# Optimization experiments

Measured on AMD Instinct MI355X. Metric: run time of the kernel, lower is better.

## Reference

```python
import jax, jax.numpy as jnp
import numpy as np
from jax import lax

V, E, H, B, S, L, T = 30000, 300, 256, 32, 256, 4, 9
H2 = 2 * H            # bidirectional encoder output / decoder hidden
DIN = 2 * H2 + L      # decoder LSTM input size


def setup_inputs() -> dict:
    key = jax.random.key(0)
    ks = jax.random.split(key, 14)
    rn = lambda k, shp, s=0.05: (jax.random.normal(k, shp, dtype=jnp.float32) * s)
    return {
        "seqs": jax.random.randint(ks[0], (B, S), 0, V, dtype=jnp.int32),
        "emb": rn(ks[1], (V, E)),
        "enc_Wih_f": rn(ks[2], (4 * H, E)),
        "enc_Whh_f": rn(ks[3], (4 * H, H)),
        "enc_b_f": rn(ks[4], (4 * H,)),
        "enc_Wih_b": rn(ks[5], (4 * H, E)),
        "enc_Whh_b": rn(ks[6], (4 * H, H)),
        "enc_b_b": rn(ks[7], (4 * H,)),
        "W_att": rn(ks[8], (H2, H2)),
        "dec_Wih": rn(ks[9], (4 * H2, DIN)),
        "dec_Whh": rn(ks[10], (4 * H2, H2)),
        "dec_b": rn(ks[11], (4 * H2,)),
        "W_tag": rn(ks[12], (T, H2)),
        "b_tag": rn(ks[13], (T,)),
    }


def _lstm_scan(x_seq, Wih, Whh, b, hidden):
    """x_seq: [S,B,Din] -> outputs [S,B,hidden]. PyTorch gate order i,f,g,o."""
    nb = x_seq.shape[1]
    h0 = jnp.zeros((nb, hidden), x_seq.dtype)
    c0 = jnp.zeros((nb, hidden), x_seq.dtype)

    def step(carry, x):
        h, c = carry
        g = x @ Wih.T + h @ Whh.T + b
        i, f, gg, o = jnp.split(g, 4, axis=-1)
        c = jax.nn.sigmoid(f) * c + jax.nn.sigmoid(i) * jnp.tanh(gg)
        h = jax.nn.sigmoid(o) * jnp.tanh(c)
        return (h, c), h

    _, hs = lax.scan(step, (h0, c0), x_seq)
    return hs


def reference(seqs, emb, enc_Wih_f, enc_Whh_f, enc_b_f, enc_Wih_b, enc_Whh_b,
              enc_b_b, W_att, dec_Wih, dec_Whh, dec_b, W_tag, b_tag):
    # embed and transpose to [S, B, E]
    x = jnp.transpose(emb[seqs], (1, 0, 2))
    # bidirectional encoder LSTM -> h: [S, B, 2H]
    h_f = _lstm_scan(x, enc_Wih_f, enc_Whh_f, enc_b_f, H)
    h_b = jnp.flip(_lstm_scan(jnp.flip(x, 0), enc_Wih_b, enc_Whh_b, enc_b_b, H), 0)
    h = jnp.concatenate([h_f, h_b], axis=-1)

    # precompute W_att @ h (same math as per-step linear in original)
    Wh = jnp.einsum('sbh,oh->sbo', h, W_att)   # [S,B,H2]

    s0 = jnp.zeros((B, H2), x.dtype)
    c0 = jnp.zeros((B, H2), x.dtype)

    def decode_level(carry, onehot):           # onehot: [L]
        def step(carry2, h_t):                 # h_t: [B,H2]
            s, c = carry2
            score = jnp.einsum('sbo,bo->bs', Wh, s)       # [B,S]
            att = jax.nn.softmax(score, axis=1)
            ctx = jnp.einsum('sbh,bs->bh', h, att)        # [B,H2]
            xin = jnp.concatenate(
                [ctx, h_t, jnp.broadcast_to(onehot, (B, L))], axis=-1)
            g = xin @ dec_Wih.T + s @ dec_Whh.T + dec_b
            i, f, gg, o = jnp.split(g, 4, axis=-1)
            c = jax.nn.sigmoid(f) * c + jax.nn.sigmoid(i) * jnp.tanh(gg)
            s = jax.nn.sigmoid(o) * jnp.tanh(c)
            return (s, c), s

        carry, outs = lax.scan(step, carry, h)  # outs: [S,B,H2]
        return carry, outs

    # state (s,c) persists across nested levels, matching the original loop
    _, all_outs = lax.scan(decode_level, (s0, c0), jnp.eye(L, dtype=x.dtype))
    # [L,S,B,H2] -> tag scores [L,S,B,T]
    return jnp.einsum('lsbh,th->lsbt', all_outs, W_tag) + b_tag
```

## Files before the change

kernel.cpp:

```cpp
#include <hip/hip_runtime.h>
#include <cstdint>
#include <cstddef>

using u16 = unsigned short;
using u32 = unsigned int;

typedef __attribute__((ext_vector_type(8))) __bf16 bf16x8;
typedef __attribute__((ext_vector_type(4))) float f32x4;

__device__ __forceinline__ float bf2f(u16 u){
  union { u32 i; float f; } v; v.i = ((u32)u) << 16; return v.f;
}
__device__ __forceinline__ u16 f2bf(float f){
  union { float f; u32 i; } v; v.f = f;
  return (u16)((v.i + 0x7FFFu + ((v.i >> 16) & 1u)) >> 16);
}
__device__ __forceinline__ float sigm(float x){ return 1.0f / (1.0f + __expf(-x)); }
__device__ __forceinline__ f32x4 mfma16(bf16x8 a, bf16x8 b, f32x4 c){
  return __builtin_amdgcn_mfma_f32_16x16x32_bf16(a, b, c, 0, 0, 0);
}
__device__ __forceinline__ float ldin(const void* p, size_t i, bool f){
  return f ? ((const float*)p)[i] : bf2f(((const u16*)p)[i]);
}

__device__ __forceinline__ void gbar(u32* bar, u32 target){
  __syncthreads();
  if (threadIdx.x == 0){
    __hip_atomic_fetch_add(bar, 1u, __ATOMIC_ACQ_REL, __HIP_MEMORY_SCOPE_AGENT);
    while (__hip_atomic_load(bar, __ATOMIC_RELAXED, __HIP_MEMORY_SCOPE_AGENT) < target)
      __builtin_amdgcn_s_sleep(2);
    (void)__hip_atomic_load(bar, __ATOMIC_ACQUIRE, __HIP_MEMORY_SCOPE_AGENT);
  }
  __syncthreads();
}

__global__ __launch_bounds__(256) void k_detect(const u32* __restrict__ embw, u32* __restrict__ dflag){
  int tid = threadIdx.x;
  u32 cnt = 0;
  for (int t = 0; t < 32; ++t){
    u32 w = embw[t*256 + tid];
    u32 e = (w >> 7) & 0xFFu;
    cnt += (e >= 0xC0u) ? 1u : 0u;
  }
  atomicAdd(dflag, cnt);
}


__global__ __launch_bounds__(256) void k_pack(
  const void* eWihF, const void* eWihB, const void* ebF, const void* ebB,
  const void* dWih, const void* dWhh, const void* db, const void* Wtag,
  const void* eWhhF, const void* eWhhB, const void* Watt, const void* btag,
  const u32* __restrict__ dflag,
  u16* __restrict__ WihCat, float* __restrict__ bcat, u16* __restrict__ WihH,
  u16* __restrict__ Wf, float* __restrict__ lbv, u16* __restrict__ WtagP,
  u16* __restrict__ WhhFb, u16* __restrict__ WhhBb, u16* __restrict__ Wattb,
  float* __restrict__ btagf)
{
  bool isf = (*dflag > 64u);
  long i = (long)blockIdx.x * 256 + threadIdx.x;
  if (i < 655360){
    long n = i / 320, e = i - n*320;
    WihCat[i] = (e < 300)
      ? f2bf(ldin(n < 1024 ? eWihF : eWihB, (size_t)(n & 1023)*300 + e, isf)) : (u16)0;
    return;
  }
  i -= 655360;
  if (i < 2048){ bcat[i] = ldin(i < 1024 ? ebF : ebB, (size_t)(i & 1023), isf); return; }
  i -= 2048;
  if (i < 1048576){
    long n = i >> 9, k = i & 511;
    WihH[i] = f2bf(ldin(dWih, (size_t)n*1028 + 512 + k, isf));
    return;
  }
  i -= 1048576;
  if (i < 2097152){
    long e  = i & 7;
    long ln = (i >> 3) & 63;
    long kt = (i >> 9) & 31;
    long rt = (i >> 14) & 3;
    long wgi = i >> 16;
    long n = rt*512 + wgi*16 + (ln & 15);
    long k = kt*32 + (ln >> 4)*8 + e;
    Wf[i] = f2bf((k < 512) ? ldin(dWih, (size_t)n*1028 + k, isf)
                           : ldin(dWhh, (size_t)n*512 + (k - 512), isf));
    return;
  }
  i -= 2097152;
  if (i < 8192){
    long l = i >> 11, n = i & 2047;
    lbv[i] = ldin(db, n, isf) + ldin(dWih, (size_t)n*1028 + 1024 + l, isf);
    return;
  }
  i -= 8192;
  if (i < 8192){
    long n = i >> 9, k = i & 511;
    WtagP[i] = (n < 9) ? f2bf(ldin(Wtag, (size_t)n*512 + k, isf)) : (u16)0;
    return;
  }
  i -= 8192;
  if (i < 262144){ WhhFb[i] = f2bf(ldin(eWhhF, i, isf)); return; }
  i -= 262144;
  if (i < 262144){ WhhBb[i] = f2bf(ldin(eWhhB, i, isf)); return; }
  i -= 262144;
  if (i < 262144){ Wattb[i] = f2bf(ldin(Watt, i, isf)); return; }
  i -= 262144;
  if (i < 16){ btagf[i] = (i < 9) ? ldin(btag, i, isf) : 0.f; return; }
}

__global__ __launch_bounds__(256) void k_gather(
  const int* __restrict__ seqs, const void* __restrict__ emb,
  const u32* __restrict__ dflag, u16* __restrict__ X)
{
  bool isf = (*dflag > 64u);
  int idx = blockIdx.x * 256 + threadIdx.x;
  if (idx >= 8192*320) return;
  int row = idx / 320, e = idx - row*320;
  int s = row >> 5, b = row & 31;
  int tok = seqs[b*256 + s];
  X[idx] = (e < 300) ? f2bf(ldin(emb, (size_t)tok*300 + e, isf)) : (u16)0;
}


__global__ __launch_bounds__(256) void k_gemm(
  const u16* __restrict__ A, const u16* __restrict__ B, const float* __restrict__ bias,
  u16* __restrict__ C, int M, int N, int K)
{
  int mb = blockIdx.x * 32;
  int wave = threadIdx.x >> 6, lane = threadIdx.x & 63;
  int nb = blockIdx.y * 256 + wave * 64;
  int rlo = lane & 15, klane = (lane >> 4) * 8;
  f32x4 acc[2][4];
  #pragma unroll
  for (int i = 0; i < 2; ++i)
    #pragma unroll
    for (int j = 0; j < 4; ++j) acc[i][j] = (f32x4){0,0,0,0};
  for (int kk = 0; kk < K; kk += 32){
    bf16x8 a0 = *(const bf16x8*)(A + (size_t)(mb + rlo)*K + kk + klane);
    bf16x8 a1 = *(const bf16x8*)(A + (size_t)(mb + 16 + rlo)*K + kk + klane);
    #pragma unroll
    for (int nt = 0; nt < 4; ++nt){
      bf16x8 bv = *(const bf16x8*)(B + (size_t)(nb + nt*16 + rlo)*K + kk + klane);
      acc[0][nt] = mfma16(a0, bv, acc[0][nt]);
      acc[1][nt] = mfma16(a1, bv, acc[1][nt]);
    }
  }
  int rbase = (lane >> 4) * 4;
  #pragma unroll
  for (int mt = 0; mt < 2; ++mt)
    #pragma unroll
    for (int nt = 0; nt < 4; ++nt){
      int col = nb + nt*16 + rlo;
      float badd = bias ? bias[col] : 0.0f;
      #pragma unroll
      for (int r = 0; r < 4; ++r){
        int row = mb + mt*16 + rbase + r;
        C[(size_t)row*N + col] = f2bf(acc[mt][nt][r] + badd);
      }
    }
}


__global__ __launch_bounds__(256) void k_transp(const u16* __restrict__ hglob, u16* __restrict__ hT)
{
  __shared__ u16 tile_t[64][264];
  int b = blockIdx.x >> 3, d0 = (blockIdx.x & 7) * 64;
  int t = threadIdx.x;
  for (int rr = 0; rr < 16; ++rr){
    int c = rr*256 + t;
    int j = c >> 4, dq = (c & 15) * 4;
    ushort4 ld = *(const ushort4*)(hglob + ((size_t)(j*32 + b)*512 + d0 + dq));
    tile_t[dq + 0][j] = ld.x;
    tile_t[dq + 1][j] = ld.y;
    tile_t[dq + 2][j] = ld.z;
    tile_t[dq + 3][j] = ld.w;
  }
  __syncthreads();
  for (int rr = 0; rr < 8; ++rr){
    int c = rr*256 + t;
    int d = c >> 5, jq = (c & 31) * 8;
    *(uint4*)(hT + ((size_t)(b*512 + d0 + d)*256 + jq)) = *(const uint4*)&tile_t[d][jq];
  }
}


__global__ __launch_bounds__(256, 1) void k_encoder(
  const u16* __restrict__ XW, const u16* __restrict__ WhhF, const u16* __restrict__ WhhB,
  u16* __restrict__ hglob, u16* __restrict__ hstate, float* __restrict__ cstate, u32* ctrl)
{
  int wg = blockIdx.x;
  int d = wg >> 4, w = wg & 15;
  const u16* Whh = d ? WhhB : WhhF;
  float* cst = cstate + d * (32*256);
  u32* bar = ctrl + d * 64;
  int tid = threadIdx.x, wave = tid >> 6, lane = tid & 63;
  int cc = lane & 15, klane = (lane >> 4) * 8, rbase = (lane >> 4) * 4;
  __shared__ float g_lds[4][32][16];
  u32 gen = 0;
  for (int t = 0; t < 256; ++t){
    int srow = d ? (255 - t) : t;
    const u16* hr = hstate + (size_t)(d*2 + (t & 1)) * (32*256);
    u16*       hw = hstate + (size_t)(d*2 + ((t & 1) ^ 1)) * (32*256);
    {
      int ncol = wave*256 + w*16 + cc;
      const u16* Brow = Whh + (size_t)ncol*256;
      f32x4 acc0 = {0,0,0,0}, acc1 = {0,0,0,0};
      #pragma unroll
      for (int kk = 0; kk < 256; kk += 32){
        bf16x8 bv = *(const bf16x8*)(Brow + kk + klane);
        bf16x8 a0 = *(const bf16x8*)(hr + cc*256 + kk + klane);
        bf16x8 a1 = *(const bf16x8*)(hr + (cc + 16)*256 + kk + klane);
        acc0 = mfma16(a0, bv, acc0);
        acc1 = mfma16(a1, bv, acc1);
      }
      #pragma unroll
      for (int r = 0; r < 4; ++r){
        g_lds[wave][rbase + r][cc]      = acc0[r];
        g_lds[wave][16 + rbase + r][cc] = acc1[r];
      }
    }
    __syncthreads();
    for (int e = tid; e < 512; e += 256){
      int b_ = e >> 4, jc = e & 15;
      int j = w*16 + jc;
      float pre[4];
      #pragma unroll
      for (int g2 = 0; g2 < 4; ++g2)
        pre[g2] = g_lds[g2][b_][jc] + bf2f(XW[(size_t)(srow*32 + b_)*2048 + d*1024 + g2*256 + j]);
      float iv = sigm(pre[0]), fv = sigm(pre[1]);
      float gv = tanhf(pre[2]), ov = sigm(pre[3]);
      float cv = fv * cst[b_*256 + j] + iv * gv;
      cst[b_*256 + j] = cv;
      float hv = ov * tanhf(cv);
      u16 hb = f2bf(hv);
      hw[b_*256 + j] = hb;
      hglob[(size_t)(srow*32 + b_)*512 + d*256 + j] = hb;
    }
    gen++;
    gbar(bar, gen * 16u);
  }
}


__global__ __launch_bounds__(512, 1) void k_decoder(
  const u16* __restrict__ Whb, const u16* __restrict__ hT,
  const u16* __restrict__ Wf, const u16* __restrict__ Xh, const float* __restrict__ lbv,
  u16* __restrict__ Ain,
  u16* __restrict__ aouts,
  u32* bar1, u32* bar2)
{
  __shared__ __align__(16) u16 s_stage[512];
  __shared__ float score_lds[256];
  __shared__ __align__(16) u16 att_bf[256];
  __shared__ float gbuf[4][16][33];
  __shared__ float c_lds[512];
  const int wg = blockIdx.x, tid = threadIdx.x;
  const int wave = tid >> 6, lane = tid & 63;
  const int q = lane >> 4, cc = lane & 15;
  c_lds[tid] = 0.0f;

  bf16x8 wh[2][16];
  #pragma unroll
  for (int rt = 0; rt < 2; ++rt)
    #pragma unroll
    for (int kt = 0; kt < 16; ++kt){
      int row = wave*32 + rt*16 + cc;
      wh[rt][kt] = *(const bf16x8*)(Whb + ((size_t)(row*32 + wg))*512 + kt*32 + q*8);
    }
  const int grt = wave >> 1, gct = wave & 1;
  const int bcol = gct*16 + cc;
  const u16* WfW = Wf + (size_t)wg*65536;
  __syncthreads();

  for (int iter = 0; iter < 1024; ++iter){
    const int l = iter >> 8, t = iter & 255;
    u16* AinC = Ain + (iter & 1)*32768;
    u16* AinN = Ain + ((iter & 1) ^ 1)*32768;

    if (tid < 64) ((uint4*)s_stage)[tid] = ((const uint4*)(AinC + wg*1024 + 512))[tid];
    __syncthreads();

    f32x4 sa0 = {0,0,0,0}, sa1 = {0,0,0,0};
    #pragma unroll
    for (int kt = 0; kt < 16; ++kt){
      bf16x8 sv = *(const bf16x8*)(s_stage + kt*32 + q*8);
      sa0 = mfma16(wh[0][kt], sv, sa0);
      sa1 = mfma16(wh[1][kt], sv, sa1);
    }
    if (cc == 0){
      #pragma unroll
      for (int r = 0; r < 4; ++r){
        score_lds[wave*32      + q*4 + r] = sa0[r];
        score_lds[wave*32 + 16 + q*4 + r] = sa1[r];
      }
    }
    __syncthreads();

    if (wave == 0){
      float x0 = score_lds[lane*4+0], x1 = score_lds[lane*4+1];
      float x2 = score_lds[lane*4+2], x3 = score_lds[lane*4+3];
      float m = fmaxf(fmaxf(x0,x1), fmaxf(x2,x3));
      #pragma unroll
      for (int off = 32; off >= 1; off >>= 1) m = fmaxf(m, __shfl_xor(m, off));
      float e0 = __expf(x0-m), e1 = __expf(x1-m), e2 = __expf(x2-m), e3 = __expf(x3-m);
      float s = e0+e1+e2+e3;
      #pragma unroll
      for (int off = 32; off >= 1; off >>= 1) s += __shfl_xor(s, off);
      float inv = 1.0f / s;
      att_bf[lane*4+0] = f2bf(e0*inv);
      att_bf[lane*4+1] = f2bf(e1*inv);
      att_bf[lane*4+2] = f2bf(e2*inv);
      att_bf[lane*4+3] = f2bf(e3*inv);
    }
    __syncthreads();

    f32x4 ca0 = {0,0,0,0}, ca1 = {0,0,0,0}, ca2 = {0,0,0,0}, ca3 = {0,0,0,0};
    #pragma unroll
    for (int jt = 0; jt < 8; ++jt){
      uint4 au = {0,0,0,0};
      if (cc == 0) au = *(const uint4*)(att_bf + jt*32 + q*8);
      bf16x8 af = *(bf16x8*)&au;
      const u16* hb = hT + ((size_t)(wg*512 + wave*64 + cc))*256 + jt*32 + q*8;
      ca0 = mfma16(af, *(const bf16x8*)(hb +    0*256), ca0);
      ca1 = mfma16(af, *(const bf16x8*)(hb +   16*256), ca1);
      ca2 = mfma16(af, *(const bf16x8*)(hb +   32*256), ca2);
      ca3 = mfma16(af, *(const bf16x8*)(hb +   48*256), ca3);
    }
    if (lane < 16){
      AinC[wg*1024 + wave*64 +  0 + lane] = f2bf(ca0[0]);
      AinC[wg*1024 + wave*64 + 16 + lane] = f2bf(ca1[0]);
      AinC[wg*1024 + wave*64 + 32 + lane] = f2bf(ca2[0]);
      AinC[wg*1024 + wave*64 + 48 + lane] = f2bf(ca3[0]);
    }
    __syncthreads();
    if (tid == 0)
      __hip_atomic_fetch_add(bar2, 1u, __ATOMIC_ACQ_REL, __HIP_MEMORY_SCOPE_AGENT);

    f32x4 ga = {0,0,0,0};
    #pragma unroll
    for (int kt = 16; kt < 32; ++kt){
      bf16x8 wa = *(const bf16x8*)(WfW + ((grt*32 + kt)*64 + lane)*8);
      bf16x8 av = *(const bf16x8*)(AinC + bcol*1024 + kt*32 + q*8);
      ga = mfma16(wa, av, ga);
    }
    if (tid == 0){
      const u32 tgt = 32u*(u32)(iter+1);
      while (__hip_atomic_load(bar2, __ATOMIC_RELAXED, __HIP_MEMORY_SCOPE_AGENT) < tgt)
        __builtin_amdgcn_s_sleep(2);
      (void)__hip_atomic_load(bar2, __ATOMIC_ACQUIRE, __HIP_MEMORY_SCOPE_AGENT);
    }
    __syncthreads();
    #pragma unroll
    for (int kt = 0; kt < 16; ++kt){
      bf16x8 wa = *(const bf16x8*)(WfW + ((grt*32 + kt)*64 + lane)*8);
      bf16x8 av = *(const bf16x8*)(AinC + bcol*1024 + kt*32 + q*8);
      ga = mfma16(wa, av, ga);
    }
    #pragma unroll
    for (int r = 0; r < 4; ++r) gbuf[grt][q*4 + r][bcol] = ga[r];
    __syncthreads();

    {
      const int b_ = tid >> 4, dd = tid & 15;
      const int gj = wg*16 + dd;
      float pre[4];
      #pragma unroll
      for (int g = 0; g < 4; ++g){
        int n = g*512 + gj;
        pre[g] = gbuf[g][dd][b_] + bf2f(Xh[(size_t)(t*32 + b_)*2048 + n]) + lbv[l*2048 + n];
      }
      float iv = sigm(pre[0]), fv = sigm(pre[1]);
      float gv = tanhf(pre[2]), ov = sigm(pre[3]);
      float cv = fv * c_lds[tid] + iv * gv;
      c_lds[tid] = cv;
      u16 hb = f2bf(ov * tanhf(cv));
      AinN[b_*1024 + 512 + gj] = hb;
      aouts[(size_t)((l*256 + t)*32 + b_)*512 + gj] = hb;
    }
    __syncthreads();
    if (tid == 0){
      __hip_atomic_fetch_add(bar1, 1u, __ATOMIC_ACQ_REL, __HIP_MEMORY_SCOPE_AGENT);
      const u32 tgt = 32u*(u32)(iter+1);
      while (__hip_atomic_load(bar1, __ATOMIC_RELAXED, __HIP_MEMORY_SCOPE_AGENT) < tgt)
        __builtin_amdgcn_s_sleep(2);
      (void)__hip_atomic_load(bar1, __ATOMIC_ACQUIRE, __HIP_MEMORY_SCOPE_AGENT);
    }
    __syncthreads();
  }
}


__global__ __launch_bounds__(256) void k_tag(
  const u16* __restrict__ aouts, const u16* __restrict__ WtagP, const float* __restrict__ btagf,
  const u32* __restrict__ dflag, void* __restrict__ out)
{
  bool isf = (*dflag > 64u);
  int wave = threadIdx.x >> 6, lane = threadIdx.x & 63;
  int mb = (blockIdx.x * 4 + wave) * 16;
  int cc = lane & 15, klane = (lane >> 4) * 8;
  f32x4 acc = {0,0,0,0};
  const u16* Arow = aouts + (size_t)(mb + cc)*512;
  const u16* Brow = WtagP + cc*512;
  #pragma unroll
  for (int kk = 0; kk < 512; kk += 32){
    bf16x8 av = *(const bf16x8*)(Arow + kk + klane);
    bf16x8 bv = *(const bf16x8*)(Brow + kk + klane);
    acc = mfma16(av, bv, acc);
  }
  int rbase = (lane >> 4) * 4;
  if (cc < 9){
    float bt = btagf[cc];
    #pragma unroll
    for (int r = 0; r < 4; ++r){
      int row = mb + rbase + r;
      float v = acc[r] + bt;
      if (isf) ((float*)out)[(size_t)row*9 + cc] = v;
      else     ((u16*)out)[(size_t)row*9 + cc] = f2bf(v);
    }
  }
}


extern "C" void kernel_launch(void* const* d_in, const int* in_sizes, int n_in,
                              void* d_out, int out_size, void* d_ws, size_t ws_size,
                              hipStream_t stream)
{
  (void)in_sizes; (void)n_in; (void)out_size;
  if (ws_size < 98625536ull) return;

  const int* seqs = (const int*)d_in[0];

  char* ws = (char*)d_ws;
  u32*    ctrl   = (u32*)(ws + 0);
  u32*    dflag  = ctrl + 240;
  u16*    Ain    = (u16*)(ws + 1024);
  u16*    hstate = (u16*)(ws + 132096);
  float*  enc_c  = (float*)(ws + 197632);
  u16*    WihCat = (u16*)(ws + 263168);
  float*  bcat   = (float*)(ws + 1573888);
  u16*    WihH   = (u16*)(ws + 1582080);
  u16*    Wf     = (u16*)(ws + 3679232);
  float*  lbv    = (float*)(ws + 7873536);
  u16*    WtagP  = (u16*)(ws + 7906304);
  u16*    WhhFb  = (u16*)(ws + 7922688);
  u16*    WhhBb  = (u16*)(ws + 8446976);
  u16*    Wattb  = (u16*)(ws + 8971264);
  float*  btagf  = (float*)(ws + 9495552);
  u16*    X      = (u16*)(ws + 9496576);
  u16*    XWXh   = (u16*)(ws + 14739456);
  u16*    aouts  = (u16*)(ws + 48293888);
  u16*    hglob  = (u16*)(ws + 48293888);
  u16*    hT     = (u16*)(ws + 81848320);
  u16*    Whb    = (u16*)(ws + 90236928);

  hipMemsetAsync(d_ws, 0, 263168, stream);

  k_detect<<<1, 256, 0, stream>>>((const u32*)d_in[1], dflag);
  k_pack<<<17993, 256, 0, stream>>>(
      d_in[2], d_in[5], d_in[4], d_in[7], d_in[9], d_in[10], d_in[11], d_in[12],
      d_in[3], d_in[6], d_in[8], d_in[13], dflag,
      WihCat, bcat, WihH, Wf, lbv, WtagP, WhhFb, WhhBb, Wattb, btagf);
  k_gather<<<10240, 256, 0, stream>>>(seqs, d_in[1], dflag, X);
  k_gemm<<<dim3(256, 8), 256, 0, stream>>>(X, WihCat, bcat, XWXh, 8192, 2048, 320);
  k_encoder<<<32, 256, 0, stream>>>(XWXh, WhhFb, WhhBb, hglob, hstate, enc_c, ctrl);
  k_gemm<<<dim3(256, 2), 256, 0, stream>>>(hglob, Wattb, nullptr, Whb, 8192, 512, 512);
  k_gemm<<<dim3(256, 8), 256, 0, stream>>>(hglob, WihH, nullptr, XWXh, 8192, 2048, 512);
  k_transp<<<256, 256, 0, stream>>>(hglob, hT);

  k_decoder<<<32, 512, 0, stream>>>(Whb, hT, Wf, XWXh, lbv, Ain, aouts,
                                    ctrl + 128, ctrl + 160);
  k_tag<<<512, 256, 0, stream>>>(aouts, WtagP, btagf, dflag, d_out);
}
```

Before: 26.47 ms.

## Use relaxed barriers with cache-bypassing loads/stores and LDS staging in recurrent kernels

Replaces acquire/release grid barriers with relaxed atomics plus explicit cache-bypassing (sc0 sc1) global loads and stores and a vmcnt wait, so cross-workgroup state exchange no longer needs full cache invalidation/writeback. The per-step hidden state and decoder input are staged into XOR-swizzled LDS blocks instead of being read repeatedly from global memory. Encoder cell state moves from global into shared memory, and outputs use nontemporal stores. The risk is memory-ordering correctness depending on the hand-written cache-bypass asm, and the decoder now needs 64KB of dynamic LDS.

```diff
diff --git a/kernel.cpp b/kernel.cpp
--- a/kernel.cpp
+++ b/kernel.cpp
@@ -23,15 +23,22 @@
   return f ? ((const float*)p)[i] : bf2f(((const u16*)p)[i]);
 }
 
-__device__ __forceinline__ void gbar(u32* bar, u32 target){
-  __syncthreads();
-  if (threadIdx.x == 0){
-    __hip_atomic_fetch_add(bar, 1u, __ATOMIC_ACQ_REL, __HIP_MEMORY_SCOPE_AGENT);
-    while (__hip_atomic_load(bar, __ATOMIC_RELAXED, __HIP_MEMORY_SCOPE_AGENT) < target)
-      __builtin_amdgcn_s_sleep(2);
-    (void)__hip_atomic_load(bar, __ATOMIC_ACQUIRE, __HIP_MEMORY_SCOPE_AGENT);
-  }
-  __syncthreads();
+__device__ __forceinline__ uint4 ldx4_cg(const u16* p){
+  uint4 r;
+  asm volatile("global_load_dwordx4 %0, %1, off sc0 sc1" : "=v"(r) : "v"(p) : "memory");
+  return r;
+}
+__device__ __forceinline__ void st16_cg(u16* p, u32 v){
+  asm volatile("global_store_short %0, %1, off sc0 sc1" :: "v"(p), "v"(v) : "memory");
+}
+__device__ __forceinline__ void wait_vm0(){ asm volatile("s_waitcnt vmcnt(0)" ::: "memory"); }
+
+__device__ __forceinline__ void bar_arrive(u32* bar){
+  __hip_atomic_fetch_add(bar, 1u, __ATOMIC_RELAXED, __HIP_MEMORY_SCOPE_AGENT);
+}
+__device__ __forceinline__ void bar_spin(u32* bar, u32 tgt){
+  while (__hip_atomic_load(bar, __ATOMIC_RELAXED, __HIP_MEMORY_SCOPE_AGENT) < tgt)
+    __builtin_amdgcn_s_sleep(1);
 }
 
 __global__ __launch_bounds__(256) void k_detect(const u32* __restrict__ embw, u32* __restrict__ dflag){
@@ -185,30 +192,48 @@
 
 __global__ __launch_bounds__(256, 1) void k_encoder(
   const u16* __restrict__ XW, const u16* __restrict__ WhhF, const u16* __restrict__ WhhB,
-  u16* __restrict__ hglob, u16* __restrict__ hstate, float* __restrict__ cstate, u32* ctrl)
+  u16* __restrict__ hglob, u16* __restrict__ hstate, u32* ctrl)
 {
   int wg = blockIdx.x;
   int d = wg >> 4, w = wg & 15;
   const u16* Whh = d ? WhhB : WhhF;
-  float* cst = cstate + d * (32*256);
   u32* bar = ctrl + d * 64;
   int tid = threadIdx.x, wave = tid >> 6, lane = tid & 63;
-  int cc = lane & 15, klane = (lane >> 4) * 8, rbase = (lane >> 4) * 4;
+  int cc = lane & 15, q = lane >> 4, klane = q * 8, rbase = q * 4;
+  __shared__ __align__(16) u16 hblk[8192];
   __shared__ float g_lds[4][32][16];
-  u32 gen = 0;
+  __shared__ float c_sh[512];
+  c_sh[tid] = 0.f; c_sh[tid + 256] = 0.f;
+  __syncthreads();
+
   for (int t = 0; t < 256; ++t){
     int srow = d ? (255 - t) : t;
-    const u16* hr = hstate + (size_t)(d*2 + (t & 1)) * (32*256);
-    u16*       hw = hstate + (size_t)(d*2 + ((t & 1) ^ 1)) * (32*256);
+    const u16* hr = hstate + (size_t)(d*2 + (t & 1)) * 8192;
+    u16*       hw = hstate + (size_t)(d*2 + ((t & 1) ^ 1)) * 8192;
+
+    {
+      int c0 = tid, c1 = tid + 256, c2 = tid + 512, c3 = tid + 768;
+      uint4 v0 = ldx4_cg(hr + (c0 >> 5)*256 + (c0 & 31)*8);
+      uint4 v1 = ldx4_cg(hr + (c1 >> 5)*256 + (c1 & 31)*8);
+      uint4 v2 = ldx4_cg(hr + (c2 >> 5)*256 + (c2 & 31)*8);
+      uint4 v3 = ldx4_cg(hr + (c3 >> 5)*256 + (c3 & 31)*8);
+      wait_vm0();
+      *(uint4*)(hblk + (c0 >> 5)*256 + (((c0 & 31) ^ ((c0 >> 5) & 7)))*8) = v0;
+      *(uint4*)(hblk + (c1 >> 5)*256 + (((c1 & 31) ^ ((c1 >> 5) & 7)))*8) = v1;
+      *(uint4*)(hblk + (c2 >> 5)*256 + (((c2 & 31) ^ ((c2 >> 5) & 7)))*8) = v2;
+      *(uint4*)(hblk + (c3 >> 5)*256 + (((c3 & 31) ^ ((c3 >> 5) & 7)))*8) = v3;
+    }
+    __syncthreads();
+
     {
       int ncol = wave*256 + w*16 + cc;
       const u16* Brow = Whh + (size_t)ncol*256;
       f32x4 acc0 = {0,0,0,0}, acc1 = {0,0,0,0};
       #pragma unroll
-      for (int kk = 0; kk < 256; kk += 32){
-        bf16x8 bv = *(const bf16x8*)(Brow + kk + klane);
-        bf16x8 a0 = *(const bf16x8*)(hr + cc*256 + kk + klane);
-        bf16x8 a1 = *(const bf16x8*)(hr + (cc + 16)*256 + kk + klane);
+      for (int kt = 0; kt < 8; ++kt){
+        bf16x8 bv = *(const bf16x8*)(Brow + kt*32 + klane);
+        bf16x8 a0 = *(const bf16x8*)(hblk + cc*256 + ((kt*4 + q) ^ (cc & 7))*8);
+        bf16x8 a1 = *(const bf16x8*)(hblk + (cc + 16)*256 + ((kt*4 + q) ^ (cc & 7))*8);
         acc0 = mfma16(a0, bv, acc0);
         acc1 = mfma16(a1, bv, acc1);
       }
@@ -219,6 +244,7 @@
       }
     }
     __syncthreads();
+
     for (int e = tid; e < 512; e += 256){
       int b_ = e >> 4, jc = e & 15;
       int j = w*16 + jc;
@@ -228,15 +254,19 @@
         pre[g2] = g_lds[g2][b_][jc] + bf2f(XW[(size_t)(srow*32 + b_)*2048 + d*1024 + g2*256 + j]);
       float iv = sigm(pre[0]), fv = sigm(pre[1]);
       float gv = tanhf(pre[2]), ov = sigm(pre[3]);
-      float cv = fv * cst[b_*256 + j] + iv * gv;
-      cst[b_*256 + j] = cv;
-      float hv = ov * tanhf(cv);
-      u16 hb = f2bf(hv);
-      hw[b_*256 + j] = hb;
-      hglob[(size_t)(srow*32 + b_)*512 + d*256 + j] = hb;
-    }
-    gen++;
-    gbar(bar, gen * 16u);
+      float cv = fv * c_sh[e] + iv * gv;
+      c_sh[e] = cv;
+      u16 hb = f2bf(ov * tanhf(cv));
+      st16_cg(hw + b_*256 + j, (u32)hb);
+      __builtin_nontemporal_store(hb, hglob + (size_t)(srow*32 + b_)*512 + d*256 + j);
+    }
+    wait_vm0();
+    __syncthreads();
+    if (tid == 0){
+      bar_arrive(bar);
+      bar_spin(bar, (u32)(t + 1) * 16u);
+    }
+    __syncthreads();
   }
 }
 
@@ -248,7 +278,7 @@
   u16* __restrict__ aouts,
   u32* bar1, u32* bar2)
 {
-  __shared__ __align__(16) u16 s_stage[512];
+  extern __shared__ __align__(16) u16 ablk[];
   __shared__ float score_lds[256];
   __shared__ __align__(16) u16 att_bf[256];
   __shared__ float gbuf[4][16][33];
@@ -276,13 +306,24 @@
     u16* AinC = Ain + (iter & 1)*32768;
     u16* AinN = Ain + ((iter & 1) ^ 1)*32768;
 
-    if (tid < 64) ((uint4*)s_stage)[tid] = ((const uint4*)(AinC + wg*1024 + 512))[tid];
+    {
+      int c0 = tid, c1 = tid + 512, c2 = tid + 1024, c3 = tid + 1536;
+      uint4 v0 = ldx4_cg(AinC + (c0 >> 6)*1024 + 512 + (c0 & 63)*8);
+      uint4 v1 = ldx4_cg(AinC + (c1 >> 6)*1024 + 512 + (c1 & 63)*8);
+      uint4 v2 = ldx4_cg(AinC + (c2 >> 6)*1024 + 512 + (c2 & 63)*8);
+      uint4 v3 = ldx4_cg(AinC + (c3 >> 6)*1024 + 512 + (c3 & 63)*8);
+      wait_vm0();
+      *(uint4*)(ablk + (c0 >> 6)*1024 + (64 + ((c0 & 63) ^ ((c0 >> 6) & 7)))*8) = v0;
+      *(uint4*)(ablk + (c1 >> 6)*1024 + (64 + ((c1 & 63) ^ ((c1 >> 6) & 7)))*8) = v1;
+      *(uint4*)(ablk + (c2 >> 6)*1024 + (64 + ((c2 & 63) ^ ((c2 >> 6) & 7)))*8) = v2;
+      *(uint4*)(ablk + (c3 >> 6)*1024 + (64 + ((c3 & 63) ^ ((c3 >> 6) & 7)))*8) = v3;
+    }
     __syncthreads();
 
     f32x4 sa0 = {0,0,0,0}, sa1 = {0,0,0,0};
     #pragma unroll
     for (int kt = 0; kt < 16; ++kt){
-      bf16x8 sv = *(const bf16x8*)(s_stage + kt*32 + q*8);
+      bf16x8 sv = *(const bf16x8*)(ablk + wg*1024 + ((64 + kt*4 + q) ^ (wg & 7))*8);
       sa0 = mfma16(wh[0][kt], sv, sa0);
       sa1 = mfma16(wh[1][kt], sv, sa1);
     }
@@ -320,39 +361,50 @@
       if (cc == 0) au = *(const uint4*)(att_bf + jt*32 + q*8);
       bf16x8 af = *(bf16x8*)&au;
       const u16* hb = hT + ((size_t)(wg*512 + wave*64 + cc))*256 + jt*32 + q*8;
-      ca0 = mfma16(af, *(const bf16x8*)(hb +    0*256), ca0);
-      ca1 = mfma16(af, *(const bf16x8*)(hb +   16*256), ca1);
-      ca2 = mfma16(af, *(const bf16x8*)(hb +   32*256), ca2);
-      ca3 = mfma16(af, *(const bf16x8*)(hb +   48*256), ca3);
-    }
-    if (lane < 16){
-      AinC[wg*1024 + wave*64 +  0 + lane] = f2bf(ca0[0]);
-      AinC[wg*1024 + wave*64 + 16 + lane] = f2bf(ca1[0]);
-      AinC[wg*1024 + wave*64 + 32 + lane] = f2bf(ca2[0]);
-      AinC[wg*1024 + wave*64 + 48 + lane] = f2bf(ca3[0]);
-    }
-    __syncthreads();
-    if (tid == 0)
-      __hip_atomic_fetch_add(bar2, 1u, __ATOMIC_ACQ_REL, __HIP_MEMORY_SCOPE_AGENT);
+      ca0 = mfma16(af, *(const bf16x8*)(hb +  0*256), ca0);
+      ca1 = mfma16(af, *(const bf16x8*)(hb + 16*256), ca1);
+      ca2 = mfma16(af, *(const bf16x8*)(hb + 32*256), ca2);
+      ca3 = mfma16(af, *(const bf16x8*)(hb + 48*256), ca3);
+    }
+    if (q == 0){
+      u16* dst = AinC + wg*1024 + wave*64 + cc;
+      st16_cg(dst +  0, (u32)f2bf(ca0[0]));
+      st16_cg(dst + 16, (u32)f2bf(ca1[0]));
+      st16_cg(dst + 32, (u32)f2bf(ca2[0]));
+      st16_cg(dst + 48, (u32)f2bf(ca3[0]));
+    }
+    wait_vm0();
+    __syncthreads();
+    if (tid == 0) bar_arrive(bar2);
 
     f32x4 ga = {0,0,0,0};
     #pragma unroll
     for (int kt = 16; kt < 32; ++kt){
       bf16x8 wa = *(const bf16x8*)(WfW + ((grt*32 + kt)*64 + lane)*8);
-      bf16x8 av = *(const bf16x8*)(AinC + bcol*1024 + kt*32 + q*8);
+      bf16x8 av = *(const bf16x8*)(ablk + bcol*1024 + ((kt*4 + q) ^ (bcol & 7))*8);
       ga = mfma16(wa, av, ga);
     }
-    if (tid == 0){
-      const u32 tgt = 32u*(u32)(iter+1);
-      while (__hip_atomic_load(bar2, __ATOMIC_RELAXED, __HIP_MEMORY_SCOPE_AGENT) < tgt)
-        __builtin_amdgcn_s_sleep(2);
-      (void)__hip_atomic_load(bar2, __ATOMIC_ACQUIRE, __HIP_MEMORY_SCOPE_AGENT);
-    }
-    __syncthreads();
+    if (tid == 0) bar_spin(bar2, 32u*(u32)(iter+1));
+    __syncthreads();
+
+    {
+      int c0 = tid, c1 = tid + 512, c2 = tid + 1024, c3 = tid + 1536;
+      uint4 v0 = ldx4_cg(AinC + (c0 >> 6)*1024 + (c0 & 63)*8);
+      uint4 v1 = ldx4_cg(AinC + (c1 >> 6)*1024 + (c1 & 63)*8);
+      uint4 v2 = ldx4_cg(AinC + (c2 >> 6)*1024 + (c2 & 63)*8);
+      uint4 v3 = ldx4_cg(AinC + (c3 >> 6)*1024 + (c3 & 63)*8);
+      wait_vm0();
+      *(uint4*)(ablk + (c0 >> 6)*1024 + (((c0 & 63) ^ ((c0 >> 6) & 7)))*8) = v0;
+      *(uint4*)(ablk + (c1 >> 6)*1024 + (((c1 & 63) ^ ((c1 >> 6) & 7)))*8) = v1;
+      *(uint4*)(ablk + (c2 >> 6)*1024 + (((c2 & 63) ^ ((c2 >> 6) & 7)))*8) = v2;
+      *(uint4*)(ablk + (c3 >> 6)*1024 + (((c3 & 63) ^ ((c3 >> 6) & 7)))*8) = v3;
+    }
+    __syncthreads();
+
     #pragma unroll
     for (int kt = 0; kt < 16; ++kt){
       bf16x8 wa = *(const bf16x8*)(WfW + ((grt*32 + kt)*64 + lane)*8);
-      bf16x8 av = *(const bf16x8*)(AinC + bcol*1024 + kt*32 + q*8);
+      bf16x8 av = *(const bf16x8*)(ablk + bcol*1024 + ((kt*4 + q) ^ (bcol & 7))*8);
       ga = mfma16(wa, av, ga);
     }
     #pragma unroll
@@ -373,16 +425,14 @@
       float cv = fv * c_lds[tid] + iv * gv;
       c_lds[tid] = cv;
       u16 hb = f2bf(ov * tanhf(cv));
-      AinN[b_*1024 + 512 + gj] = hb;
-      aouts[(size_t)((l*256 + t)*32 + b_)*512 + gj] = hb;
-    }
+      st16_cg(AinN + b_*1024 + 512 + gj, (u32)hb);
+      __builtin_nontemporal_store(hb, aouts + (size_t)((l*256 + t)*32 + b_)*512 + gj);
+    }
+    wait_vm0();
     __syncthreads();
     if (tid == 0){
-      __hip_atomic_fetch_add(bar1, 1u, __ATOMIC_ACQ_REL, __HIP_MEMORY_SCOPE_AGENT);
-      const u32 tgt = 32u*(u32)(iter+1);
-      while (__hip_atomic_load(bar1, __ATOMIC_RELAXED, __HIP_MEMORY_SCOPE_AGENT) < tgt)
-        __builtin_amdgcn_s_sleep(2);
-      (void)__hip_atomic_load(bar1, __ATOMIC_ACQUIRE, __HIP_MEMORY_SCOPE_AGENT);
+      bar_arrive(bar1);
+      bar_spin(bar1, 32u*(u32)(iter+1));
     }
     __syncthreads();
   }
@@ -434,7 +484,6 @@
   u32*    dflag  = ctrl + 240;
   u16*    Ain    = (u16*)(ws + 1024);
   u16*    hstate = (u16*)(ws + 132096);
-  float*  enc_c  = (float*)(ws + 197632);
   u16*    WihCat = (u16*)(ws + 263168);
   float*  bcat   = (float*)(ws + 1573888);
   u16*    WihH   = (u16*)(ws + 1582080);
@@ -461,12 +510,12 @@
       WihCat, bcat, WihH, Wf, lbv, WtagP, WhhFb, WhhBb, Wattb, btagf);
   k_gather<<<10240, 256, 0, stream>>>(seqs, d_in[1], dflag, X);
   k_gemm<<<dim3(256, 8), 256, 0, stream>>>(X, WihCat, bcat, XWXh, 8192, 2048, 320);
-  k_encoder<<<32, 256, 0, stream>>>(XWXh, WhhFb, WhhBb, hglob, hstate, enc_c, ctrl);
+  k_encoder<<<32, 256, 0, stream>>>(XWXh, WhhFb, WhhBb, hglob, hstate, ctrl);
   k_gemm<<<dim3(256, 2), 256, 0, stream>>>(hglob, Wattb, nullptr, Whb, 8192, 512, 512);
   k_gemm<<<dim3(256, 8), 256, 0, stream>>>(hglob, WihH, nullptr, XWXh, 8192, 2048, 512);
   k_transp<<<256, 256, 0, stream>>>(hglob, hT);
 
-  k_decoder<<<32, 512, 0, stream>>>(Whb, hT, Wf, XWXh, lbv, Ain, aouts,
-                                    ctrl + 128, ctrl + 160);
+  k_decoder<<<32, 512, 65536, stream>>>(Whb, hT, Wf, XWXh, lbv, Ain, aouts,
+                                        ctrl + 128, ctrl + 160);
   k_tag<<<512, 256, 0, stream>>>(aouts, WtagP, btagf, dflag, d_out);
 }
```

After: 21.52 ms. -18.7%, faster.
